# Performance work log

Hardware: AMD Instinct MI355X
Metric: run time of the kernel (lower is better)

The kernel has to match this reference:

```python
import jax, jax.numpy as jnp
import numpy as np

N_NODES = 100000
N_EDGES = 1600000
H, D = 4, 16          # num_heads, output_dim_node
DE = 16               # hidden_dim_edge
DIN_N = 64            # input_dim_node == H*D -> identity residual
DIN_E = 64            # input_dim_edge


def setup_inputs() -> dict:
    key = jax.random.key(0)
    ks = jax.random.split(key, 9)
    return {
        "inputs_node": jax.random.normal(ks[0], (N_NODES, DIN_N), dtype=jnp.float32),
        "inputs_edge": jax.random.normal(ks[1], (N_EDGES, DIN_E), dtype=jnp.float32),
        "src": jax.random.randint(ks[2], (N_EDGES,), 0, N_NODES, dtype=jnp.int32),
        "dst": jax.random.randint(ks[3], (N_EDGES,), 0, N_NODES, dtype=jnp.int32),
        "W_node": jax.random.normal(ks[4], (DIN_N, H * D), dtype=jnp.float32) * (1.0 / np.sqrt(DIN_N)),
        "W_edge": jax.random.normal(ks[5], (DIN_E, H * DE), dtype=jnp.float32) * (1.0 / np.sqrt(DIN_E)),
        "attn_query": jax.random.normal(ks[6], (H, D), dtype=jnp.float32) * (1.0 / np.sqrt(D)),
        "attn_key": jax.random.normal(ks[7], (H, D), dtype=jnp.float32) * (1.0 / np.sqrt(D)),
        "attn_edge": jax.random.normal(ks[8], (H, DE), dtype=jnp.float32) * (1.0 / np.sqrt(DE)),
        "bias": jnp.zeros((H * D,), dtype=jnp.float32),
    }


def reference(inputs_node, inputs_edge, src, dst, W_node, W_edge,
              attn_query, attn_key, attn_edge, bias):
    n = inputs_node.shape[0]
    hn = (inputs_node @ W_node).reshape(n, H, D)          # [N,H,D] node values
    he = (inputs_edge @ W_edge).reshape(-1, H, DE)         # [E,H,De]
    w_q = jnp.einsum("nhd,hd->nh", hn, attn_query)         # [N,H]
    w_k = jnp.einsum("nhd,hd->nh", hn, attn_key)           # [N,H]
    w_e = jnp.einsum("ehd,hd->eh", he, attn_edge)          # [E,H]
    # per-edge logits: key(src) + query(dst) + edge, then leaky_relu (torch default slope 0.01)
    logits = jax.nn.leaky_relu(w_k[src] + w_q[dst] + w_e, negative_slope=0.01)  # [E,H]
    # edge softmax segmented by destination node
    seg_max = jax.ops.segment_max(logits, dst, num_segments=n)  # [N,H]
    seg_max = jnp.where(jnp.isfinite(seg_max), seg_max, 0.0)    # empty segments -> 0
    ex = jnp.exp(logits - seg_max[dst])                          # [E,H]
    denom = jax.ops.segment_sum(ex, dst, num_segments=n)         # [N,H]
    attn = ex / denom[dst]                                       # [E,H]
    # weighted scatter-sum of source values
    msg = hn[src] * attn[:, :, None]                             # [E,H,D]
    out = jax.ops.segment_sum(msg, dst, num_segments=n)          # [N,H,D]
    out = out.reshape(n, H * D) + bias
    # activation=None -> identity; residual: input_dim_node == H*D -> identity
    out = out + inputs_node
    return out
```

## Files before the change

### kernel.cpp

```cpp
#include <hip/hip_runtime.h>


__global__ __launch_bounds__(1024) void zero_counts(int* __restrict__ p, int n) {
  int i = blockIdx.x * 1024 + threadIdx.x;
  if (i < n) p[i] = 0;
}

__global__ __launch_bounds__(256) void fold_kernel(
    const float* __restrict__ Wn, const float* __restrict__ We,
    const float* __restrict__ aq, const float* __restrict__ ak,
    const float* __restrict__ ae,
    float* __restrict__ qv, float* __restrict__ kv, float* __restrict__ ev) {
  int t = threadIdx.x;
  int j = t >> 2, h = t & 3;
  float sq = 0.f, sk = 0.f, se = 0.f;
#pragma unroll
  for (int d = 0; d < 16; d++) {
    float wn = Wn[j * 64 + h * 16 + d];
    float we = We[j * 64 + h * 16 + d];
    sq += wn * aq[h * 16 + d];
    sk += wn * ak[h * 16 + d];
    se += we * ae[h * 16 + d];
  }
  qv[t] = sq;
  kv[t] = sk;
  ev[t] = se;
}

__global__ __launch_bounds__(256) void node_proj(
    const float* __restrict__ xin, const float* __restrict__ W,
    const float* __restrict__ aq, const float* __restrict__ ak,
    float* __restrict__ hn, float* __restrict__ wq, float* __restrict__ wk,
    int n) {
  int node = blockIdx.x * blockDim.x + threadIdx.x;
  if (node >= n) return;
  const float4* xr = (const float4*)(xin + (size_t)node * 64);
  float x[64];
#pragma unroll
  for (int i = 0; i < 16; i++) {
    float4 v = xr[i];
    x[4 * i] = v.x; x[4 * i + 1] = v.y; x[4 * i + 2] = v.z; x[4 * i + 3] = v.w;
  }
  float q[4] = {0, 0, 0, 0}, kk[4] = {0, 0, 0, 0};
  float4* ho = (float4*)(hn + (size_t)node * 64);
  for (int c4 = 0; c4 < 16; c4++) {
    float a0 = 0, a1 = 0, a2 = 0, a3 = 0;
#pragma unroll
    for (int j = 0; j < 64; j++) {
      const float4 wv = *(const float4*)(W + j * 64 + c4 * 4);
      a0 += x[j] * wv.x; a1 += x[j] * wv.y; a2 += x[j] * wv.z; a3 += x[j] * wv.w;
    }
    float4 aqv = *(const float4*)(aq + c4 * 4);
    float4 akv = *(const float4*)(ak + c4 * 4);
    int h = c4 >> 2;
    q[h]  += a0 * aqv.x + a1 * aqv.y + a2 * aqv.z + a3 * aqv.w;
    kk[h] += a0 * akv.x + a1 * akv.y + a2 * akv.z + a3 * akv.w;
    float4 o; o.x = a0; o.y = a1; o.z = a2; o.w = a3;
    ho[c4] = o;
  }
  *(float4*)(wq + (size_t)node * 4) = make_float4(q[0], q[1], q[2], q[3]);
  *(float4*)(wk + (size_t)node * 4) = make_float4(kk[0], kk[1], kk[2], kk[3]);
}

__global__ __launch_bounds__(256) void hist_kernel(
    const int* __restrict__ dst, int* __restrict__ counts, int e) {
  int i = blockIdx.x * blockDim.x + threadIdx.x;
  if (i < e) atomicAdd(&counts[dst[i]], 1);
}

__global__ __launch_bounds__(1024) void scan_block(
    const int* __restrict__ counts, int* __restrict__ excl,
    int* __restrict__ bsum, int n) {
  __shared__ int wsum[16];
  int i = blockIdx.x * 1024 + threadIdx.x;
  int v = (i < n) ? counts[i] : 0;
  int x = v;
#pragma unroll
  for (int o = 1; o < 64; o <<= 1) {
    int y = __shfl_up(x, o, 64);
    if ((threadIdx.x & 63) >= o) x += y;
  }
  int wid = threadIdx.x >> 6;
  if ((threadIdx.x & 63) == 63) wsum[wid] = x;
  __syncthreads();
  if (threadIdx.x < 16) {
    int s = wsum[threadIdx.x];
#pragma unroll
    for (int o = 1; o < 16; o <<= 1) {
      int y = __shfl_up(s, o, 16);
      if ((int)threadIdx.x >= o) s += y;
    }
    wsum[threadIdx.x] = s;
  }
  __syncthreads();
  int base = (wid > 0) ? wsum[wid - 1] : 0;
  int incl = base + x;
  if (i < n) excl[i] = incl - v;
  if (threadIdx.x == 1023) bsum[blockIdx.x] = incl;
}

__global__ __launch_bounds__(128) void scan_bsum(int* __restrict__ bsum, int nb) {
  __shared__ int ws[2];
  int t = threadIdx.x;
  int v = (t < nb) ? bsum[t] : 0;
  int x = v;
#pragma unroll
  for (int o = 1; o < 64; o <<= 1) {
    int y = __shfl_up(x, o, 64);
    if ((t & 63) >= o) x += y;
  }
  if ((t & 63) == 63) ws[t >> 6] = x;
  __syncthreads();
  int base = (t >= 64) ? ws[0] : 0;
  int incl = base + x;
  if (t < nb) bsum[t] = incl - v;
}

__global__ __launch_bounds__(1024) void scan_add(
    int* __restrict__ excl, const int* __restrict__ bsumExcl,
    int* __restrict__ cursor, int n, int total) {
  int i = blockIdx.x * 1024 + threadIdx.x;
  if (i < n) {
    int off = excl[i] + bsumExcl[blockIdx.x];
    excl[i] = off;
    cursor[i] = off;
  }
  if (blockIdx.x == 0 && threadIdx.x == 0) excl[n] = total;
}

__global__ __launch_bounds__(256) void edge_logits(
    const float* __restrict__ xe, const int* __restrict__ src,
    const int* __restrict__ dst, const float* __restrict__ ev,
    const float* __restrict__ wq, const float* __restrict__ wk,
    float4* __restrict__ ex, int E) {
  int e = blockIdx.x * blockDim.x + threadIdx.x;
  if (e >= E) return;
  const float4* row = (const float4*)(xe + (size_t)e * 64);
  float w0 = 0, w1 = 0, w2 = 0, w3 = 0;
#pragma unroll
  for (int j4 = 0; j4 < 16; j4++) {
    float4 xv = row[j4];
    const float4 e0 = *(const float4*)(ev + (j4 * 4 + 0) * 4);
    const float4 e1 = *(const float4*)(ev + (j4 * 4 + 1) * 4);
    const float4 e2 = *(const float4*)(ev + (j4 * 4 + 2) * 4);
    const float4 e3 = *(const float4*)(ev + (j4 * 4 + 3) * 4);
    w0 += xv.x * e0.x + xv.y * e1.x + xv.z * e2.x + xv.w * e3.x;
    w1 += xv.x * e0.y + xv.y * e1.y + xv.z * e2.y + xv.w * e3.y;
    w2 += xv.x * e0.z + xv.y * e1.z + xv.z * e2.z + xv.w * e3.z;
    w3 += xv.x * e0.w + xv.y * e1.w + xv.z * e2.w + xv.w * e3.w;
  }
  int s = src[e], d = dst[e];
  float4 kv4 = *(const float4*)(wk + (size_t)s * 4);
  float4 qv4 = *(const float4*)(wq + (size_t)d * 4);
  float l0 = kv4.x + qv4.x + w0;
  float l1 = kv4.y + qv4.y + w1;
  float l2 = kv4.z + qv4.z + w2;
  float l3 = kv4.w + qv4.w + w3;
  l0 = l0 > 0.f ? l0 : 0.01f * l0;
  l1 = l1 > 0.f ? l1 : 0.01f * l1;
  l2 = l2 > 0.f ? l2 : 0.01f * l2;
  l3 = l3 > 0.f ? l3 : 0.01f * l3;
  ex[e] = make_float4(__expf(l0), __expf(l1), __expf(l2), __expf(l3));
}

__global__ __launch_bounds__(256) void permute_kernel(
    const int* __restrict__ src, const int* __restrict__ dst,
    int* __restrict__ cursor, int2* __restrict__ csr_pair, int E) {
  int e = blockIdx.x * blockDim.x + threadIdx.x;
  if (e >= E) return;
  int d = dst[e];
  int pos = atomicAdd(&cursor[d], 1);
  csr_pair[pos] = make_int2(src[e], e);
}

__global__ __launch_bounds__(256) void aggregate(
    const int* __restrict__ offsets, const int2* __restrict__ csr_pair,
    const float* __restrict__ ex, const float* __restrict__ hn,
    const float* __restrict__ xin, const float* __restrict__ bias,
    float* __restrict__ out, int n) {
  int t = threadIdx.x;
  int lane = t & 63;
  int node = blockIdx.x * 4 + (t >> 6);
  if (node >= n) return;
  int h = lane >> 4;
  int start = offsets[node], end = offsets[node + 1];
  float den0 = 0.f, den1 = 0.f, acc0 = 0.f, acc1 = 0.f;
  int i = start;
  for (; i + 8 <= end; i += 8) {
    int2 p0 = csr_pair[i + 0], p1 = csr_pair[i + 1];
    int2 p2 = csr_pair[i + 2], p3 = csr_pair[i + 3];
    int2 p4 = csr_pair[i + 4], p5 = csr_pair[i + 5];
    int2 p6 = csr_pair[i + 6], p7 = csr_pair[i + 7];
    float x0 = ex[(size_t)p0.y * 4 + h], x1 = ex[(size_t)p1.y * 4 + h];
    float x2 = ex[(size_t)p2.y * 4 + h], x3 = ex[(size_t)p3.y * 4 + h];
    float x4 = ex[(size_t)p4.y * 4 + h], x5 = ex[(size_t)p5.y * 4 + h];
    float x6 = ex[(size_t)p6.y * 4 + h], x7 = ex[(size_t)p7.y * 4 + h];
    float v0 = hn[(size_t)p0.x * 64 + lane], v1 = hn[(size_t)p1.x * 64 + lane];
    float v2 = hn[(size_t)p2.x * 64 + lane], v3 = hn[(size_t)p3.x * 64 + lane];
    float v4 = hn[(size_t)p4.x * 64 + lane], v5 = hn[(size_t)p5.x * 64 + lane];
    float v6 = hn[(size_t)p6.x * 64 + lane], v7 = hn[(size_t)p7.x * 64 + lane];
    den0 += (x0 + x2) + (x4 + x6);
    den1 += (x1 + x3) + (x5 + x7);
    acc0 += x0 * v0; acc1 += x1 * v1;
    acc0 += x2 * v2; acc1 += x3 * v3;
    acc0 += x4 * v4; acc1 += x5 * v5;
    acc0 += x6 * v6; acc1 += x7 * v7;
  }
  for (; i < end; i++) {
    int2 p = csr_pair[i];
    float x = ex[(size_t)p.y * 4 + h];
    float v = hn[(size_t)p.x * 64 + lane];
    den0 += x;
    acc0 += x * v;
  }
  float den = den0 + den1, acc = acc0 + acc1;
  float r = (end > start) ? acc / den : 0.f;
  out[(size_t)node * 64 + lane] = r + bias[lane] + xin[(size_t)node * 64 + lane];
}

extern "C" void kernel_launch(void* const* d_in, const int* in_sizes, int n_in,
                              void* d_out, int out_size, void* d_ws, size_t ws_size,
                              hipStream_t stream) {
  const float* xn  = (const float*)d_in[0];
  const float* xe  = (const float*)d_in[1];
  const int*   src = (const int*)d_in[2];
  const int*   dst = (const int*)d_in[3];
  const float* Wn  = (const float*)d_in[4];
  const float* We  = (const float*)d_in[5];
  const float* aq  = (const float*)d_in[6];
  const float* ak  = (const float*)d_in[7];
  const float* ae  = (const float*)d_in[8];
  const float* bias = (const float*)d_in[9];
  float* out = (float*)d_out;

  const int n = in_sizes[0] / 64;
  const int E = in_sizes[2];

  size_t off = 0;
  auto carve = [&](size_t bytes) {
    size_t p = off;
    off = (off + bytes + 255) & ~(size_t)255;
    return p;
  };
  char* ws = (char*)d_ws;
  size_t o_hn    = carve((size_t)n * 64 * 4);
  size_t o_wq    = carve((size_t)n * 4 * 4);
  size_t o_wk    = carve((size_t)n * 4 * 4);
  size_t o_qv    = carve(256 * 4);
  size_t o_kv    = carve(256 * 4);
  size_t o_ev    = carve(256 * 4);
  size_t o_cnt   = carve((size_t)n * 4);
  size_t o_offs  = carve((size_t)(n + 1) * 4);
  size_t o_cur   = carve((size_t)n * 4);
  size_t o_bsum  = carve(1024 * 4);
  size_t o_pair  = carve((size_t)E * 8);
  size_t o_ex    = carve((size_t)E * 16);
  if (off > ws_size) return;

  float* hn      = (float*)(ws + o_hn);
  float* wq      = (float*)(ws + o_wq);
  float* wk      = (float*)(ws + o_wk);
  float* qv      = (float*)(ws + o_qv);
  float* kv      = (float*)(ws + o_kv);
  float* ev      = (float*)(ws + o_ev);
  int*   counts  = (int*)(ws + o_cnt);
  int*   offsets = (int*)(ws + o_offs);
  int*   cursor  = (int*)(ws + o_cur);
  int*   bsum    = (int*)(ws + o_bsum);
  int2*  csr_pair = (int2*)(ws + o_pair);
  float4* ex     = (float4*)(ws + o_ex);

  const int NB = (n + 1023) / 1024;
  if (NB > 128) return;

  zero_counts<<<NB, 1024, 0, stream>>>(counts, n);
  fold_kernel<<<1, 256, 0, stream>>>(Wn, We, aq, ak, ae, qv, kv, ev);
  node_proj<<<(n + 255) / 256, 256, 0, stream>>>(xn, Wn, aq, ak, hn, wq, wk, n);
  hist_kernel<<<(E + 255) / 256, 256, 0, stream>>>(dst, counts, E);
  scan_block<<<NB, 1024, 0, stream>>>(counts, offsets, bsum, n);
  scan_bsum<<<1, 128, 0, stream>>>(bsum, NB);
  scan_add<<<NB, 1024, 0, stream>>>(offsets, bsum, cursor, n, E);
  edge_logits<<<(E + 255) / 256, 256, 0, stream>>>(
      xe, src, dst, ev, wq, wk, ex, E);
  permute_kernel<<<(E + 255) / 256, 256, 0, stream>>>(
      src, dst, cursor, csr_pair, E);
  aggregate<<<(n + 3) / 4, 256, 0, stream>>>(
      offsets, csr_pair, (const float*)ex, hn, xn, bias, out, n);
}
```

Baseline: 492.1 us.

## Fuse edge logit computation into the CSR aggregation kernel

Removes the separate per-edge logits kernel and its E×4 float intermediate buffer. Each wavefront now handles four edges at a time: it gathers the edge feature rows by original edge id, reduces the projected logits with lane shuffles, applies leaky-relu and exp, and accumulates the weighted source values in the same loop. This avoids writing and then re-reading the exp buffer and saves one kernel launch. In exchange, edge rows are read in random order, and each iteration is a longer chain of dependent loads and shuffles with less unrolling than the old aggregate loop.

```diff
diff --git a/kernel.cpp b/kernel.cpp
--- a/kernel.cpp
+++ b/kernel.cpp
@@ -128,41 +128,6 @@
   if (blockIdx.x == 0 && threadIdx.x == 0) excl[n] = total;
 }
 
-__global__ __launch_bounds__(256) void edge_logits(
-    const float* __restrict__ xe, const int* __restrict__ src,
-    const int* __restrict__ dst, const float* __restrict__ ev,
-    const float* __restrict__ wq, const float* __restrict__ wk,
-    float4* __restrict__ ex, int E) {
-  int e = blockIdx.x * blockDim.x + threadIdx.x;
-  if (e >= E) return;
-  const float4* row = (const float4*)(xe + (size_t)e * 64);
-  float w0 = 0, w1 = 0, w2 = 0, w3 = 0;
-#pragma unroll
-  for (int j4 = 0; j4 < 16; j4++) {
-    float4 xv = row[j4];
-    const float4 e0 = *(const float4*)(ev + (j4 * 4 + 0) * 4);
-    const float4 e1 = *(const float4*)(ev + (j4 * 4 + 1) * 4);
-    const float4 e2 = *(const float4*)(ev + (j4 * 4 + 2) * 4);
-    const float4 e3 = *(const float4*)(ev + (j4 * 4 + 3) * 4);
-    w0 += xv.x * e0.x + xv.y * e1.x + xv.z * e2.x + xv.w * e3.x;
-    w1 += xv.x * e0.y + xv.y * e1.y + xv.z * e2.y + xv.w * e3.y;
-    w2 += xv.x * e0.z + xv.y * e1.z + xv.z * e2.z + xv.w * e3.z;
-    w3 += xv.x * e0.w + xv.y * e1.w + xv.z * e2.w + xv.w * e3.w;
-  }
-  int s = src[e], d = dst[e];
-  float4 kv4 = *(const float4*)(wk + (size_t)s * 4);
-  float4 qv4 = *(const float4*)(wq + (size_t)d * 4);
-  float l0 = kv4.x + qv4.x + w0;
-  float l1 = kv4.y + qv4.y + w1;
-  float l2 = kv4.z + qv4.z + w2;
-  float l3 = kv4.w + qv4.w + w3;
-  l0 = l0 > 0.f ? l0 : 0.01f * l0;
-  l1 = l1 > 0.f ? l1 : 0.01f * l1;
-  l2 = l2 > 0.f ? l2 : 0.01f * l2;
-  l3 = l3 > 0.f ? l3 : 0.01f * l3;
-  ex[e] = make_float4(__expf(l0), __expf(l1), __expf(l2), __expf(l3));
-}
-
 __global__ __launch_bounds__(256) void permute_kernel(
     const int* __restrict__ src, const int* __restrict__ dst,
     int* __restrict__ cursor, int2* __restrict__ csr_pair, int E) {
@@ -173,47 +138,69 @@
   csr_pair[pos] = make_int2(src[e], e);
 }
 
-__global__ __launch_bounds__(256) void aggregate(
+__global__ __launch_bounds__(256) void mega_aggregate(
     const int* __restrict__ offsets, const int2* __restrict__ csr_pair,
-    const float* __restrict__ ex, const float* __restrict__ hn,
-    const float* __restrict__ xin, const float* __restrict__ bias,
-    float* __restrict__ out, int n) {
+    const float* __restrict__ xe, const float* __restrict__ ev,
+    const float* __restrict__ wq, const float* __restrict__ wk,
+    const float* __restrict__ hn, const float* __restrict__ xin,
+    const float* __restrict__ bias, float* __restrict__ out, int n) {
   int t = threadIdx.x;
   int lane = t & 63;
   int node = blockIdx.x * 4 + (t >> 6);
   if (node >= n) return;
-  int h = lane >> 4;
+  int li = lane & 15;
+  int g = lane >> 4;
+  const float4* ev4 = (const float4*)ev;
+  float4 e0 = ev4[li * 4 + 0];
+  float4 e1 = ev4[li * 4 + 1];
+  float4 e2 = ev4[li * 4 + 2];
+  float4 e3 = ev4[li * 4 + 3];
+  float4 qv4 = *(const float4*)(wq + (size_t)node * 4);
+  const float4* xe4 = (const float4*)xe;
   int start = offsets[node], end = offsets[node + 1];
-  float den0 = 0.f, den1 = 0.f, acc0 = 0.f, acc1 = 0.f;
-  int i = start;
-  for (; i + 8 <= end; i += 8) {
-    int2 p0 = csr_pair[i + 0], p1 = csr_pair[i + 1];
-    int2 p2 = csr_pair[i + 2], p3 = csr_pair[i + 3];
-    int2 p4 = csr_pair[i + 4], p5 = csr_pair[i + 5];
-    int2 p6 = csr_pair[i + 6], p7 = csr_pair[i + 7];
-    float x0 = ex[(size_t)p0.y * 4 + h], x1 = ex[(size_t)p1.y * 4 + h];
-    float x2 = ex[(size_t)p2.y * 4 + h], x3 = ex[(size_t)p3.y * 4 + h];
-    float x4 = ex[(size_t)p4.y * 4 + h], x5 = ex[(size_t)p5.y * 4 + h];
-    float x6 = ex[(size_t)p6.y * 4 + h], x7 = ex[(size_t)p7.y * 4 + h];
-    float v0 = hn[(size_t)p0.x * 64 + lane], v1 = hn[(size_t)p1.x * 64 + lane];
-    float v2 = hn[(size_t)p2.x * 64 + lane], v3 = hn[(size_t)p3.x * 64 + lane];
-    float v4 = hn[(size_t)p4.x * 64 + lane], v5 = hn[(size_t)p5.x * 64 + lane];
-    float v6 = hn[(size_t)p6.x * 64 + lane], v7 = hn[(size_t)p7.x * 64 + lane];
-    den0 += (x0 + x2) + (x4 + x6);
-    den1 += (x1 + x3) + (x5 + x7);
-    acc0 += x0 * v0; acc1 += x1 * v1;
-    acc0 += x2 * v2; acc1 += x3 * v3;
-    acc0 += x4 * v4; acc1 += x5 * v5;
-    acc0 += x6 * v6; acc1 += x7 * v7;
-  }
-  for (; i < end; i++) {
-    int2 p = csr_pair[i];
-    float x = ex[(size_t)p.y * 4 + h];
-    float v = hn[(size_t)p.x * 64 + lane];
-    den0 += x;
-    acc0 += x * v;
-  }
-  float den = den0 + den1, acc = acc0 + acc1;
+  float acc = 0.f, den = 0.f;
+  for (int i = start; i < end; i += 4) {
+    int m = end - i;
+    int2 p = make_int2(0, 0);
+    if (lane < 4 && lane < m) p = csr_pair[i + lane];
+    int mysrc = __shfl(p.x, g);
+    int myeid = __shfl(p.y, g);
+    float4 xr = xe4[(size_t)myeid * 16 + li];
+    float4 part;
+    part.x = xr.x * e0.x + xr.y * e1.x + xr.z * e2.x + xr.w * e3.x;
+    part.y = xr.x * e0.y + xr.y * e1.y + xr.z * e2.y + xr.w * e3.y;
+    part.z = xr.x * e0.z + xr.y * e1.z + xr.z * e2.z + xr.w * e3.z;
+    part.w = xr.x * e0.w + xr.y * e1.w + xr.z * e2.w + xr.w * e3.w;
+#pragma unroll
+    for (int o = 1; o < 16; o <<= 1) {
+      part.x += __shfl_xor(part.x, o);
+      part.y += __shfl_xor(part.y, o);
+      part.z += __shfl_xor(part.z, o);
+      part.w += __shfl_xor(part.w, o);
+    }
+    float4 kv4 = *(const float4*)(wk + (size_t)mysrc * 4);
+    float l0 = kv4.x + qv4.x + part.x;
+    float l1 = kv4.y + qv4.y + part.y;
+    float l2 = kv4.z + qv4.z + part.z;
+    float l3 = kv4.w + qv4.w + part.w;
+    l0 = l0 > 0.f ? l0 : 0.01f * l0;
+    l1 = l1 > 0.f ? l1 : 0.01f * l1;
+    l2 = l2 > 0.f ? l2 : 0.01f * l2;
+    l3 = l3 > 0.f ? l3 : 0.01f * l3;
+    float x0 = __expf(l0), x1 = __expf(l1), x2 = __expf(l2), x3 = __expf(l3);
+    int q2 = lane & 3;
+    float tmp = (q2 == 0) ? x0 : (q2 == 1) ? x1 : (q2 == 2) ? x2 : x3;
+#pragma unroll
+    for (int e = 0; e < 4; e++) {
+      if (e < m) {
+        float exh = __shfl(tmp, (e << 4) | g);
+        int se = __shfl(p.x, e);
+        float v = hn[(size_t)se * 64 + lane];
+        acc += exh * v;
+        den += exh;
+      }
+    }
+  }
   float r = (end > start) ? acc / den : 0.f;
   out[(size_t)node * 64 + lane] = r + bias[lane] + xin[(size_t)node * 64 + lane];
 }
@@ -254,7 +241,6 @@
   size_t o_cur   = carve((size_t)n * 4);
   size_t o_bsum  = carve(1024 * 4);
   size_t o_pair  = carve((size_t)E * 8);
-  size_t o_ex    = carve((size_t)E * 16);
   if (off > ws_size) return;
 
   float* hn      = (float*)(ws + o_hn);
@@ -268,7 +254,6 @@
   int*   cursor  = (int*)(ws + o_cur);
   int*   bsum    = (int*)(ws + o_bsum);
   int2*  csr_pair = (int2*)(ws + o_pair);
-  float4* ex     = (float4*)(ws + o_ex);
 
   const int NB = (n + 1023) / 1024;
   if (NB > 128) return;
@@ -280,10 +265,8 @@
   scan_block<<<NB, 1024, 0, stream>>>(counts, offsets, bsum, n);
   scan_bsum<<<1, 128, 0, stream>>>(bsum, NB);
   scan_add<<<NB, 1024, 0, stream>>>(offsets, bsum, cursor, n, E);
-  edge_logits<<<(E + 255) / 256, 256, 0, stream>>>(
-      xe, src, dst, ev, wq, wk, ex, E);
   permute_kernel<<<(E + 255) / 256, 256, 0, stream>>>(
       src, dst, cursor, csr_pair, E);
-  aggregate<<<(n + 3) / 4, 256, 0, stream>>>(
-      offsets, csr_pair, (const float*)ex, hn, xn, bias, out, n);
-}
+  mega_aggregate<<<(n + 3) / 4, 256, 0, stream>>>(
+      offsets, csr_pair, xe, ev, wq, wk, hn, xn, bias, out, n);
+}
```

Result: slower. 558.0 us (+13.4%).
